# Kernel optimization log

Measured on AMD Instinct MI355X. Metric: run time of the kernel, lower is better.

The kernel has to match this reference:

```python
import jax, jax.numpy as jnp
import numpy as np


def gcn_conv(x, src, dst, W, b, num_nodes):
    # PyG GCNConv: add self-loops, symmetric deg^-1/2 normalization, scatter-add.
    h = x @ W                                    # [N, out]
    loops = jnp.arange(num_nodes, dtype=src.dtype)
    s = jnp.concatenate([src, loops])            # [E+N]
    d = jnp.concatenate([dst, loops])            # [E+N]
    deg = jax.ops.segment_sum(jnp.ones_like(d, dtype=h.dtype), d, num_segments=num_nodes)
    dinv = jnp.where(deg > 0, jax.lax.rsqrt(deg), 0.0)
    norm = dinv[s] * dinv[d]                     # [E+N]
    msgs = h[s] * norm[:, None]                  # gather + scale  [E+N, out]
    out = jax.ops.segment_sum(msgs, d, num_segments=num_nodes)
    return out + b


NUM_GRAPHS = 512


def setup_inputs() -> dict:
    key = jax.random.key(0)
    ks = jax.random.split(key, 12)
    N, E, F = 50000, 400000, 128
    x = jax.random.normal(ks[0], (N, F), dtype=jnp.float32)
    edge_index = jax.random.randint(ks[1], (2, E), 0, N, dtype=jnp.int64)
    batch = jnp.sort(jax.random.randint(ks[2], (N,), 0, NUM_GRAPHS, dtype=jnp.int64))
    def lin(k, fi, fo):
        return jax.random.normal(k, (fi, fo), dtype=jnp.float32) * (1.0 / np.sqrt(fi))
    return {
        "x": x, "edge_index": edge_index, "batch": batch,
        "W1": lin(ks[3], F, 512), "b1": jnp.zeros((512,), jnp.float32),
        "W2": lin(ks[4], 512, 256), "b2": jnp.zeros((256,), jnp.float32),
        "W3": lin(ks[5], 256, 128), "b3": jnp.zeros((128,), jnp.float32),
        "W4": lin(ks[6], 128, 32), "b4": jnp.zeros((32,), jnp.float32),
        "W5": lin(ks[7], 32, 10), "b5": jnp.zeros((10,), jnp.float32),
    }


def reference(x, edge_index, batch, W1, b1, W2, b2, W3, b3, W4, b4, W5, b5):
    N = x.shape[0]
    src, dst = edge_index[0], edge_index[1]
    h = gcn_conv(x, src, dst, W1, b1, N)
    h = jax.nn.leaky_relu(h, negative_slope=0.01)
    h = gcn_conv(h, src, dst, W2, b2, N)          # [N, 256]
    embs = jax.ops.segment_max(h, batch, num_segments=NUM_GRAPHS)  # [G, 256]
    z = ((h @ W3 + b3) @ W4 + b4) @ W5 + b5       # [N, 10]
    out = jax.ops.segment_max(z, batch, num_segments=NUM_GRAPHS)   # [G, 10]
    return (out, embs)
```

## Files before the change

### kernel.cpp

```cpp
#include <hip/hip_runtime.h>
#include <math.h>

#define DIV_UP(a,b) (((a)+(b)-1)/(b))

typedef __attribute__((ext_vector_type(8))) short bf16x8;
typedef __attribute__((ext_vector_type(4))) float f32x4;

__device__ inline unsigned short f2b(float x) {
    unsigned int u = __float_as_uint(x);
    u += 0x7fffu + ((u >> 16) & 1u);
    return (unsigned short)(u >> 16);
}

__device__ inline void cvt8(uint4 v, float* a) {
    a[0] = __uint_as_float(v.x << 16); a[1] = __uint_as_float(v.x & 0xffff0000u);
    a[2] = __uint_as_float(v.y << 16); a[3] = __uint_as_float(v.y & 0xffff0000u);
    a[4] = __uint_as_float(v.z << 16); a[5] = __uint_as_float(v.z & 0xffff0000u);
    a[6] = __uint_as_float(v.w << 16); a[7] = __uint_as_float(v.w & 0xffff0000u);
}

__device__ inline void gl16(void* lds, const void* g) {
    __builtin_amdgcn_global_load_lds(
        (const __attribute__((address_space(1))) void*)g,
        (__attribute__((address_space(3))) void*)lds, 16, 0, 0);
}

__global__ void k_zero_i(int* p, int n) {
    int i = blockIdx.x * blockDim.x + threadIdx.x;
    if (i < n) p[i] = 0;
}

__global__ void k_hist(const int* __restrict__ dst, int* __restrict__ hist, int E) {
    int i = blockIdx.x * blockDim.x + threadIdx.x;
    if (i < E) atomicAdd(&hist[dst[i]], 1);
}

__global__ __launch_bounds__(256) void k_scan_bsum(const int* __restrict__ hist,
                                                   int* __restrict__ bsum, int N) {
    __shared__ int red[256];
    int t = threadIdx.x;
    int base = blockIdx.x * 1024 + t * 4;
    int s = 0;
    if (base + 3 < N) {
        int4 v = *(const int4*)&hist[base];
        s = v.x + v.y + v.z + v.w;
    } else {
        for (int j = 0; j < 4; ++j) if (base + j < N) s += hist[base + j];
    }
    red[t] = s;
    __syncthreads();
    for (int off = 128; off >= 1; off >>= 1) {
        if (t < off) red[t] += red[t + off];
        __syncthreads();
    }
    if (t == 0) bsum[blockIdx.x] = red[0];
}

__global__ __launch_bounds__(1024) void k_scan_boff(const int* __restrict__ bsum,
        int* __restrict__ boff, int* __restrict__ row_off, int NB, int N) {
    __shared__ int s[1024];
    int t = threadIdx.x;
    int v = (t < NB) ? bsum[t] : 0;
    s[t] = v;
    __syncthreads();
    for (int off = 1; off < 1024; off <<= 1) {
        int u = (t >= off) ? s[t - off] : 0;
        __syncthreads();
        s[t] += u;
        __syncthreads();
    }
    if (t < NB) boff[t] = s[t] - v;
    if (t == NB - 1) row_off[N] = s[t];
}

__global__ __launch_bounds__(256) void k_scan_apply(const int* __restrict__ hist,
        const int* __restrict__ boff, int* __restrict__ row_off,
        float* __restrict__ dinv, int N) {
    __shared__ int s[256];
    int t = threadIdx.x;
    int base = blockIdx.x * 1024 + t * 4;
    int v[4];
    int loc = 0;
#pragma unroll
    for (int j = 0; j < 4; ++j) { v[j] = (base + j < N) ? hist[base + j] : 0; loc += v[j]; }
    s[t] = loc;
    __syncthreads();
    for (int off = 1; off < 256; off <<= 1) {
        int u = (t >= off) ? s[t - off] : 0;
        __syncthreads();
        s[t] += u;
        __syncthreads();
    }
    int run = boff[blockIdx.x] + s[t] - loc;
#pragma unroll
    for (int j = 0; j < 4; ++j) {
        if (base + j < N) {
            row_off[base + j] = run;
            dinv[base + j] = rsqrtf((float)(v[j] + 1));
        }
        run += v[j];
    }
}

__global__ void k_bin(const int* __restrict__ src, const int* __restrict__ dst,
                      const int* __restrict__ row_off, int* __restrict__ cursor,
                      const float* __restrict__ dinv,
                      int* __restrict__ csr_src, float* __restrict__ csr_w, int E) {
    int i = blockIdx.x * blockDim.x + threadIdx.x;
    if (i >= E) return;
    int d = dst[i], s = src[i];
    int pos = row_off[d] + atomicAdd(&cursor[d], 1);
    csr_src[pos] = s;
    csr_w[pos] = dinv[s] * dinv[d];
}

__global__ __launch_bounds__(256) void k_pre(
        const float* __restrict__ W3, const float* __restrict__ W4,
        const float* __restrict__ W5, const float* __restrict__ b3,
        const float* __restrict__ b4, const float* __restrict__ b5,
        float* __restrict__ WcT, float* __restrict__ bc,
        const int* __restrict__ batch, int* __restrict__ bounds, int N, int G, int nb,
        const float* __restrict__ x, unsigned short* __restrict__ xb, int n4,
        const float* __restrict__ W1, unsigned short* __restrict__ w1t, int K1, int N1,
        const float* __restrict__ W2, unsigned short* __restrict__ w2t, int K2, int N2) {
    int b = blockIdx.x;
    int t = threadIdx.x;
    if (b < 11) {
        int c = b;
        if (c < 10) {
            __shared__ float Tc[128];
            if (t < 128) {
                float s = 0.f;
#pragma unroll 8
                for (int k = 0; k < 32; ++k) s = fmaf(W4[t * 32 + k], W5[k * 10 + c], s);
                Tc[t] = s;
            }
            __syncthreads();
            float s = 0.f;
            const float* w3r = &W3[t * 128];
#pragma unroll 8
            for (int j = 0; j < 128; ++j) s = fmaf(w3r[j], Tc[j], s);
            WcT[c * 256 + t] = s;
        } else {
            __shared__ float v[32];
            if (t < 32) {
                float s = b4[t];
                for (int j = 0; j < 128; ++j) s = fmaf(b3[j], W4[j * 32 + t], s);
                v[t] = s;
            }
            __syncthreads();
            if (t < 10) {
                float s = b5[t];
                for (int k = 0; k < 32; ++k) s = fmaf(v[k], W5[k * 10 + t], s);
                bc[t] = s;
            }
        }
        return;
    }
    if (b < 11 + nb) {
        int g = (b - 11) * 256 + t;
        if (g > G) return;
        int lo = 0, hi = N;
        while (lo < hi) { int mid = (lo + hi) >> 1; if (batch[mid] < g) lo = mid + 1; else hi = mid; }
        bounds[g] = lo;
        return;
    }
    int i = (b - 11 - nb) * 256 + t;
    if (i < n4) {
        float4 v = ((const float4*)x)[i];
        ushort4 o;
        o.x = f2b(v.x); o.y = f2b(v.y); o.z = f2b(v.z); o.w = f2b(v.w);
        ((ushort4*)xb)[i] = o;
        return;
    }
    i -= n4;
    if (i < K1 * N1) {
        int k = i / N1, n = i % N1;
        w1t[(size_t)n * K1 + k] = f2b(W1[i]);
        return;
    }
    i -= K1 * N1;
    if (i < K2 * N2) {
        int k = i / N2, n = i % N2;
        w2t[(size_t)n * K2 + k] = f2b(W2[i]);
    }
}

template <int F>
__global__ __launch_bounds__(256) void k_gather_b(const unsigned short* __restrict__ H,
        const int* __restrict__ row_off, const int* __restrict__ csr_src,
        const float* __restrict__ csr_w, const float* __restrict__ dinv,
        const float* __restrict__ bias, unsigned short* __restrict__ outb, int N) {
    const int LPN = F / 8;
    const int NPB = 256 / LPN;
    int node = blockIdx.x * NPB + threadIdx.x / LPN;
    if (node >= N) return;
    int f = (threadIdx.x % LPN) * 8;
    const unsigned short* Hf = H + f;
    float sc = dinv[node]; sc *= sc;
    float a[8];
    cvt8(*(const uint4*)&Hf[(size_t)node * F], a);
#pragma unroll
    for (int j = 0; j < 8; ++j) a[j] *= sc;
    if (bias) {
#pragma unroll
        for (int j = 0; j < 8; ++j) a[j] += bias[f + j];
    }
    int e0 = row_off[node], e1 = row_off[node + 1];
    int e = e0;
    for (; e + 4 <= e1; e += 4) {
        int s0 = csr_src[e + 0], s1 = csr_src[e + 1];
        int s2 = csr_src[e + 2], s3 = csr_src[e + 3];
        uint4 v0 = *(const uint4*)&Hf[(size_t)s0 * F];
        uint4 v1 = *(const uint4*)&Hf[(size_t)s1 * F];
        uint4 v2 = *(const uint4*)&Hf[(size_t)s2 * F];
        uint4 v3 = *(const uint4*)&Hf[(size_t)s3 * F];
        float w0 = csr_w[e + 0], w1 = csr_w[e + 1];
        float w2 = csr_w[e + 2], w3 = csr_w[e + 3];
        float b0[8], b1[8], b2[8], b3[8];
        cvt8(v0, b0); cvt8(v1, b1); cvt8(v2, b2); cvt8(v3, b3);
#pragma unroll
        for (int j = 0; j < 8; ++j) {
            a[j] = fmaf(w0, b0[j], a[j]);
            a[j] = fmaf(w1, b1[j], a[j]);
            a[j] = fmaf(w2, b2[j], a[j]);
            a[j] = fmaf(w3, b3[j], a[j]);
        }
    }
    for (; e < e1; ++e) {
        int s = csr_src[e];
        float w = csr_w[e];
        float b[8];
        cvt8(*(const uint4*)&Hf[(size_t)s * F], b);
#pragma unroll
        for (int j = 0; j < 8; ++j) a[j] = fmaf(w, b[j], a[j]);
    }
    uint4 o;
    o.x = (unsigned)f2b(a[0]) | ((unsigned)f2b(a[1]) << 16);
    o.y = (unsigned)f2b(a[2]) | ((unsigned)f2b(a[3]) << 16);
    o.z = (unsigned)f2b(a[4]) | ((unsigned)f2b(a[5]) << 16);
    o.w = (unsigned)f2b(a[6]) | ((unsigned)f2b(a[7]) << 16);
    *(uint4*)&outb[(size_t)node * F + f] = o;
}

template <int OUT_BF16, int ACT>
__global__ __launch_bounds__(512) void k_gemm_mfma256(const unsigned short* __restrict__ A,
        const unsigned short* __restrict__ Bt, const float* __restrict__ bias,
        void* __restrict__ Cout, int M, int K, int NC) {
    __shared__ __align__(16) unsigned short As[128][64];
    __shared__ __align__(16) unsigned short Bs[256][64];
    int tid = threadIdx.x;
    int wave = tid >> 6, lane = tid & 63;
    int row0 = blockIdx.y * 128, col0 = blockIdx.x * 256;
    int wr = (wave >> 2) * 64, wc = (wave & 3) * 64;
    f32x4 acc[4][4] = {};
    int lr = lane & 15;
    int lg = lane >> 4;
    int sw = ((lane & 7) ^ (lane >> 3)) << 3;
    int ch0 = (lg ^ (lr & 7)) << 3;
    int ch1 = ch0 ^ (4 << 3);

    for (int k0 = 0; k0 < K; k0 += 64) {
#pragma unroll
        for (int c = 0; c < 2; ++c) {
            int rl = c * 64 + wave * 8 + (lane >> 3);
            int gr = min(row0 + rl, M - 1);
            gl16(&As[c * 64 + wave * 8][0], &A[(size_t)gr * K + k0 + sw]);
        }
#pragma unroll
        for (int c = 0; c < 4; ++c) {
            int rl = c * 64 + wave * 8 + (lane >> 3);
            gl16(&Bs[c * 64 + wave * 8][0], &Bt[(size_t)(col0 + rl) * K + k0 + sw]);
        }
        __syncthreads();
        bf16x8 af[2][4], bv[2][4];
#pragma unroll
        for (int i = 0; i < 4; ++i) {
            int ra = wr + i * 16 + lr;
            int rb = wc + i * 16 + lr;
            af[0][i] = *(const bf16x8*)&As[ra][ch0];
            af[1][i] = *(const bf16x8*)&As[ra][ch1];
            bv[0][i] = *(const bf16x8*)&Bs[rb][ch0];
            bv[1][i] = *(const bf16x8*)&Bs[rb][ch1];
        }
#pragma unroll
        for (int s = 0; s < 2; ++s)
#pragma unroll
            for (int i = 0; i < 4; ++i)
#pragma unroll
                for (int j = 0; j < 4; ++j)
                    acc[i][j] = __builtin_amdgcn_mfma_f32_16x16x32_bf16(bv[s][j], af[s][i], acc[i][j], 0, 0, 0);
        __syncthreads();
    }

    int q4 = lg * 4;
    float4 bb[4];
#pragma unroll
    for (int j = 0; j < 4; ++j)
        bb[j] = bias ? *(const float4*)&bias[col0 + wc + j * 16 + q4]
                     : make_float4(0.f, 0.f, 0.f, 0.f);
#pragma unroll
    for (int i = 0; i < 4; ++i) {
        int row = row0 + wr + i * 16 + lr;
        if (row >= M) continue;
#pragma unroll
        for (int j = 0; j < 4; ++j) {
            int c0 = col0 + wc + j * 16 + q4;
            float4 v;
            v.x = acc[i][j][0] + bb[j].x;
            v.y = acc[i][j][1] + bb[j].y;
            v.z = acc[i][j][2] + bb[j].z;
            v.w = acc[i][j][3] + bb[j].w;
            if (ACT) {
                v.x = (v.x >= 0.f) ? v.x : 0.01f * v.x;
                v.y = (v.y >= 0.f) ? v.y : 0.01f * v.y;
                v.z = (v.z >= 0.f) ? v.z : 0.01f * v.z;
                v.w = (v.w >= 0.f) ? v.w : 0.01f * v.w;
            }
            if (OUT_BF16) {
                uint2 o;
                o.x = (unsigned)f2b(v.x) | ((unsigned)f2b(v.y) << 16);
                o.y = (unsigned)f2b(v.z) | ((unsigned)f2b(v.w) << 16);
                *(uint2*)&((unsigned short*)Cout)[(size_t)row * NC + c0] = o;
            } else {
                *(float4*)&((float*)Cout)[(size_t)row * NC + c0] = v;
            }
        }
    }
}

__global__ __launch_bounds__(320) void k_head_segmax(const unsigned short* __restrict__ H,
        const float* __restrict__ WcT, const float* __restrict__ bc,
        const int* __restrict__ bounds, float* __restrict__ out,
        float* __restrict__ out_emb) {
    __shared__ __align__(16) float Ws[10][260];
    __shared__ float bs[10];
    __shared__ float red[320];
    int t = threadIdx.x;
    for (int i = t; i < 2560; i += 320) Ws[i / 256][i % 256] = WcT[i];
    if (t < 10) bs[t] = bc[t];
    __syncthreads();
    int g = blockIdx.x;
    int s = bounds[g], e = bounds[g + 1];
    int col = t % 10, rs = t / 10;
    float m = -INFINITY;
    for (int r = s + rs; r < e; r += 32) {
        const unsigned short* hr = &H[(size_t)r * 256];
        float acc = bs[col];
#pragma unroll 4
        for (int k = 0; k < 256; k += 8) {
            float h[8];
            cvt8(*(const uint4*)&hr[k], h);
            float4 wa = *(const float4*)&Ws[col][k];
            float4 wb = *(const float4*)&Ws[col][k + 4];
            acc = fmaf(h[0], wa.x, acc);
            acc = fmaf(h[1], wa.y, acc);
            acc = fmaf(h[2], wa.z, acc);
            acc = fmaf(h[3], wa.w, acc);
            acc = fmaf(h[4], wb.x, acc);
            acc = fmaf(h[5], wb.y, acc);
            acc = fmaf(h[6], wb.z, acc);
            acc = fmaf(h[7], wb.w, acc);
        }
        m = fmaxf(m, acc);
    }
    red[t] = m;
    __syncthreads();
    for (int step = 16; step >= 1; step >>= 1) {
        if (rs < step) red[rs * 10 + col] = fmaxf(red[rs * 10 + col], red[(rs + step) * 10 + col]);
        __syncthreads();
    }
    if (rs == 0) out[(size_t)g * 10 + col] = red[col];
    if (t < 256) {
        float mm = -INFINITY;
        for (int r = s; r < e; ++r)
            mm = fmaxf(mm, __uint_as_float(((unsigned)H[(size_t)r * 256 + t]) << 16));
        out_emb[(size_t)g * 256 + t] = mm;
    }
}

extern "C" void kernel_launch(void* const* d_in, const int* in_sizes, int n_in,
                              void* d_out, int out_size, void* d_ws, size_t ws_size,
                              hipStream_t stream) {
    const float* x  = (const float*)d_in[0];
    const int* ei   = (const int*)d_in[1];
    const int* batch= (const int*)d_in[2];
    const float* W1 = (const float*)d_in[3];
    const float* b1 = (const float*)d_in[4];
    const float* W2 = (const float*)d_in[5];
    const float* b2 = (const float*)d_in[6];
    const float* W3 = (const float*)d_in[7];
    const float* b3 = (const float*)d_in[8];
    const float* W4 = (const float*)d_in[9];
    const float* b4 = (const float*)d_in[10];
    const float* W5 = (const float*)d_in[11];
    const float* b5 = (const float*)d_in[12];

    const int N  = in_sizes[2];
    const int F  = in_sizes[0] / N;
    const int E  = in_sizes[1] / 2;
    const int C1 = in_sizes[4];
    const int C2 = in_sizes[6];
    const int C5 = in_sizes[12];
    const int G  = out_size / (C2 + C5);
    const int NB = DIV_UP(N, 1024);

    const int* srcp = ei;
    const int* dstp = ei + E;

    uintptr_t p = (uintptr_t)d_ws;
    auto carve = [&](size_t bytes) {
        uintptr_t r = p;
        p += (bytes + 255) & ~(size_t)255;
        return (void*)r;
    };
    int* hist    = (int*)carve(sizeof(int) * N);
    int* cursor  = (int*)carve(sizeof(int) * N);
    int* row_off = (int*)carve(sizeof(int) * (N + 1));
    int* bounds  = (int*)carve(sizeof(int) * (G + 1));
    int* bsum    = (int*)carve(sizeof(int) * NB);
    int* boff    = (int*)carve(sizeof(int) * NB);
    int* csr_src = (int*)carve(sizeof(int) * E);
    float* csr_w = (float*)carve(sizeof(float) * E);
    float* dinv  = (float*)carve(sizeof(float) * N);
    float* wct   = (float*)carve(sizeof(float) * C2 * C5);
    float* bcv   = (float*)carve(sizeof(float) * C5);
    unsigned short* w1t = (unsigned short*)carve(sizeof(short) * F * C1);
    unsigned short* w2t = (unsigned short*)carve(sizeof(short) * C1 * C2);
    unsigned short* xb    = (unsigned short*)carve(sizeof(short) * (size_t)N * F);
    unsigned short* aggxb = (unsigned short*)carve(sizeof(short) * (size_t)N * F);
    unsigned short* h1b   = (unsigned short*)carve(sizeof(short) * (size_t)N * C1);
    unsigned short* t2b   = (unsigned short*)carve(sizeof(short) * (size_t)N * C2);
    unsigned short* h2b   = (unsigned short*)carve(sizeof(short) * (size_t)N * C2);

    float* out     = (float*)d_out;
    float* out_emb = out + (size_t)G * C5;

    int zspan = (int)(((sizeof(int) * N + 255) & ~(size_t)255) / 4) + N;
    k_zero_i<<<DIV_UP(zspan, 256), 256, 0, stream>>>(hist, zspan);
    k_hist<<<DIV_UP(E, 256), 256, 0, stream>>>(dstp, hist, E);
    k_scan_bsum<<<NB, 256, 0, stream>>>(hist, bsum, N);
    k_scan_boff<<<1, 1024, 0, stream>>>(bsum, boff, row_off, NB, N);
    k_scan_apply<<<NB, 256, 0, stream>>>(hist, boff, row_off, dinv, N);
    k_bin<<<DIV_UP(E, 256), 256, 0, stream>>>(srcp, dstp, row_off, cursor, dinv,
                                              csr_src, csr_w, E);

    int n4 = N * F / 4;
    int nb_bounds = DIV_UP(G + 1, 256);
    int prep_total = n4 + F * C1 + C1 * C2;
    int pre_blocks = 11 + nb_bounds + DIV_UP(prep_total, 256);
    k_pre<<<pre_blocks, 256, 0, stream>>>(W3, W4, W5, b3, b4, b5, wct, bcv,
                                          batch, bounds, N, G, nb_bounds,
                                          x, xb, n4, W1, w1t, F, C1, W2, w2t, C1, C2);

    k_gather_b<128><<<DIV_UP(N, 16), 256, 0, stream>>>(
        xb, row_off, csr_src, csr_w, dinv, nullptr, aggxb, N);
    dim3 g1(C1 / 256, DIV_UP(N, 128));
    k_gemm_mfma256<1, 1><<<g1, 512, 0, stream>>>(aggxb, w1t, b1, h1b, N, F, C1);

    dim3 g2(C2 / 256, DIV_UP(N, 128));
    k_gemm_mfma256<1, 0><<<g2, 512, 0, stream>>>(h1b, w2t, nullptr, t2b, N, C1, C2);
    k_gather_b<256><<<DIV_UP(N, 8), 256, 0, stream>>>(
        t2b, row_off, csr_src, csr_w, dinv, b2, h2b, N);

    k_head_segmax<<<G, 320, 0, stream>>>(h2b, wct, bcv, bounds, out, out_emb);
}
```

Before: 286.8 us.

## Fuse second aggregation with head projection and segment-max via float atomics

Merges the layer-2 gather, the collapsed W3·W4·W5 head projection and both segment-max reductions into one kernel. Each block of 8 nodes computes h2 in registers, runs the 10-column head with shuffle reductions, and pushes per-graph maxima to the outputs with sign-aware integer atomic max/min. The separate bf16 h2 buffer write/read, the graph-bounds binary search and the per-graph head kernel are dropped, and the output is initialised to -inf in the prep kernel instead. The cost is many global atomics, each block reloading the head weights into LDS, and h2 being kept in fp32 instead of rounded to bf16, which changes numerics slightly.

```diff
diff --git a/kernel.cpp b/kernel.cpp
--- a/kernel.cpp
+++ b/kernel.cpp
@@ -17,6 +17,11 @@
     a[2] = __uint_as_float(v.y << 16); a[3] = __uint_as_float(v.y & 0xffff0000u);
     a[4] = __uint_as_float(v.z << 16); a[5] = __uint_as_float(v.z & 0xffff0000u);
     a[6] = __uint_as_float(v.w << 16); a[7] = __uint_as_float(v.w & 0xffff0000u);
+}
+
+__device__ inline void atomicMaxF(float* addr, float v) {
+    if (v >= 0.f) atomicMax((int*)addr, __float_as_int(v));
+    else          atomicMin((unsigned int*)addr, __float_as_uint(v));
 }
 
 __device__ inline void gl16(void* lds, const void* g) {
@@ -119,7 +124,7 @@
         const float* __restrict__ W5, const float* __restrict__ b3,
         const float* __restrict__ b4, const float* __restrict__ b5,
         float* __restrict__ WcT, float* __restrict__ bc,
-        const int* __restrict__ batch, int* __restrict__ bounds, int N, int G, int nb,
+        unsigned* __restrict__ outp, int nout, int nfo,
         const float* __restrict__ x, unsigned short* __restrict__ xb, int n4,
         const float* __restrict__ W1, unsigned short* __restrict__ w1t, int K1, int N1,
         const float* __restrict__ W2, unsigned short* __restrict__ w2t, int K2, int N2) {
@@ -157,15 +162,12 @@
         }
         return;
     }
-    if (b < 11 + nb) {
-        int g = (b - 11) * 256 + t;
-        if (g > G) return;
-        int lo = 0, hi = N;
-        while (lo < hi) { int mid = (lo + hi) >> 1; if (batch[mid] < g) lo = mid + 1; else hi = mid; }
-        bounds[g] = lo;
+    if (b < 11 + nfo) {
+        int i = (b - 11) * 256 + t;
+        if (i < nout) outp[i] = 0xff800000u;
         return;
     }
-    int i = (b - 11 - nb) * 256 + t;
+    int i = (b - 11 - nfo) * 256 + t;
     if (i < n4) {
         float4 v = ((const float4*)x)[i];
         ushort4 o;
@@ -241,6 +243,123 @@
     o.z = (unsigned)f2b(a[4]) | ((unsigned)f2b(a[5]) << 16);
     o.w = (unsigned)f2b(a[6]) | ((unsigned)f2b(a[7]) << 16);
     *(uint4*)&outb[(size_t)node * F + f] = o;
+}
+
+__global__ __launch_bounds__(256) void k_gather_head(
+        const unsigned short* __restrict__ H,
+        const int* __restrict__ row_off, const int* __restrict__ csr_src,
+        const float* __restrict__ csr_w, const float* __restrict__ dinv,
+        const float* __restrict__ bias, const int* __restrict__ batch,
+        const float* __restrict__ WcT, const float* __restrict__ bc,
+        float* __restrict__ out, float* __restrict__ out_emb, int N) {
+    __shared__ __align__(16) float Ws[10][260];
+    __shared__ float bs[10];
+    __shared__ __align__(16) float h2s[8][264];
+    __shared__ float zl[8][10];
+    __shared__ int gl[8];
+    int t = threadIdx.x;
+    for (int i = t; i < 2560; i += 256) Ws[i >> 8][i & 255] = WcT[i];
+    if (t < 10) bs[t] = bc[t];
+    int nl = t >> 5;
+    int q  = t & 31;
+    int node = blockIdx.x * 8 + nl;
+    bool valid = node < N;
+    if (q == 0) gl[nl] = valid ? batch[node] : -1;
+    int f = q * 8;
+    const unsigned short* Hf = H + f;
+    float a[8] = {0.f, 0.f, 0.f, 0.f, 0.f, 0.f, 0.f, 0.f};
+    if (valid) {
+        float sc = dinv[node]; sc *= sc;
+        cvt8(*(const uint4*)&Hf[(size_t)node * 256], a);
+#pragma unroll
+        for (int j = 0; j < 8; ++j) a[j] = fmaf(a[j], sc, bias[f + j]);
+        int e0 = row_off[node], e1 = row_off[node + 1];
+        int e = e0;
+        for (; e + 4 <= e1; e += 4) {
+            int s0 = csr_src[e + 0], s1 = csr_src[e + 1];
+            int s2 = csr_src[e + 2], s3 = csr_src[e + 3];
+            uint4 v0 = *(const uint4*)&Hf[(size_t)s0 * 256];
+            uint4 v1 = *(const uint4*)&Hf[(size_t)s1 * 256];
+            uint4 v2 = *(const uint4*)&Hf[(size_t)s2 * 256];
+            uint4 v3 = *(const uint4*)&Hf[(size_t)s3 * 256];
+            float w0 = csr_w[e + 0], w1 = csr_w[e + 1];
+            float w2 = csr_w[e + 2], w3 = csr_w[e + 3];
+            float b0[8], b1[8], b2v[8], b3v[8];
+            cvt8(v0, b0); cvt8(v1, b1); cvt8(v2, b2v); cvt8(v3, b3v);
+#pragma unroll
+            for (int j = 0; j < 8; ++j) {
+                a[j] = fmaf(w0, b0[j], a[j]);
+                a[j] = fmaf(w1, b1[j], a[j]);
+                a[j] = fmaf(w2, b2v[j], a[j]);
+                a[j] = fmaf(w3, b3v[j], a[j]);
+            }
+        }
+        for (; e < e1; ++e) {
+            int s = csr_src[e];
+            float w = csr_w[e];
+            float bv[8];
+            cvt8(*(const uint4*)&Hf[(size_t)s * 256], bv);
+#pragma unroll
+            for (int j = 0; j < 8; ++j) a[j] = fmaf(w, bv[j], a[j]);
+        }
+    }
+    __syncthreads();
+
+#pragma unroll
+    for (int c = 0; c < 10; ++c) {
+        float4 wa = *(const float4*)&Ws[c][f];
+        float4 wb = *(const float4*)&Ws[c][f + 4];
+        float s = a[0] * wa.x;
+        s = fmaf(a[1], wa.y, s);
+        s = fmaf(a[2], wa.z, s);
+        s = fmaf(a[3], wa.w, s);
+        s = fmaf(a[4], wb.x, s);
+        s = fmaf(a[5], wb.y, s);
+        s = fmaf(a[6], wb.z, s);
+        s = fmaf(a[7], wb.w, s);
+        s += __shfl_xor(s, 16);
+        s += __shfl_xor(s, 8);
+        s += __shfl_xor(s, 4);
+        s += __shfl_xor(s, 2);
+        s += __shfl_xor(s, 1);
+        if (q == 0) zl[nl][c] = s + bs[c];
+    }
+    *(float4*)&h2s[nl][f]     = make_float4(a[0], a[1], a[2], a[3]);
+    *(float4*)&h2s[nl][f + 4] = make_float4(a[4], a[5], a[6], a[7]);
+    __syncthreads();
+
+    {
+        int curg = -1; float m = 0.f;
+#pragma unroll
+        for (int n = 0; n < 8; ++n) {
+            int g = gl[n];
+            if (g < 0) continue;
+            float v = h2s[n][t];
+            if (g != curg) {
+                if (curg >= 0) atomicMaxF(&out_emb[(size_t)curg * 256 + t], m);
+                curg = g; m = v;
+            } else {
+                m = fmaxf(m, v);
+            }
+        }
+        if (curg >= 0) atomicMaxF(&out_emb[(size_t)curg * 256 + t], m);
+    }
+    if (t < 10) {
+        int curg = -1; float m = 0.f;
+#pragma unroll
+        for (int n = 0; n < 8; ++n) {
+            int g = gl[n];
+            if (g < 0) continue;
+            float v = zl[n][t];
+            if (g != curg) {
+                if (curg >= 0) atomicMaxF(&out[(size_t)curg * 10 + t], m);
+                curg = g; m = v;
+            } else {
+                m = fmaxf(m, v);
+            }
+        }
+        if (curg >= 0) atomicMaxF(&out[(size_t)curg * 10 + t], m);
+    }
 }
 
 template <int OUT_BF16, int ACT>
@@ -329,56 +448,6 @@
     }
 }
 
-__global__ __launch_bounds__(320) void k_head_segmax(const unsigned short* __restrict__ H,
-        const float* __restrict__ WcT, const float* __restrict__ bc,
-        const int* __restrict__ bounds, float* __restrict__ out,
-        float* __restrict__ out_emb) {
-    __shared__ __align__(16) float Ws[10][260];
-    __shared__ float bs[10];
-    __shared__ float red[320];
-    int t = threadIdx.x;
-    for (int i = t; i < 2560; i += 320) Ws[i / 256][i % 256] = WcT[i];
-    if (t < 10) bs[t] = bc[t];
-    __syncthreads();
-    int g = blockIdx.x;
-    int s = bounds[g], e = bounds[g + 1];
-    int col = t % 10, rs = t / 10;
-    float m = -INFINITY;
-    for (int r = s + rs; r < e; r += 32) {
-        const unsigned short* hr = &H[(size_t)r * 256];
-        float acc = bs[col];
-#pragma unroll 4
-        for (int k = 0; k < 256; k += 8) {
-            float h[8];
-            cvt8(*(const uint4*)&hr[k], h);
-            float4 wa = *(const float4*)&Ws[col][k];
-            float4 wb = *(const float4*)&Ws[col][k + 4];
-            acc = fmaf(h[0], wa.x, acc);
-            acc = fmaf(h[1], wa.y, acc);
-            acc = fmaf(h[2], wa.z, acc);
-            acc = fmaf(h[3], wa.w, acc);
-            acc = fmaf(h[4], wb.x, acc);
-            acc = fmaf(h[5], wb.y, acc);
-            acc = fmaf(h[6], wb.z, acc);
-            acc = fmaf(h[7], wb.w, acc);
-        }
-        m = fmaxf(m, acc);
-    }
-    red[t] = m;
-    __syncthreads();
-    for (int step = 16; step >= 1; step >>= 1) {
-        if (rs < step) red[rs * 10 + col] = fmaxf(red[rs * 10 + col], red[(rs + step) * 10 + col]);
-        __syncthreads();
-    }
-    if (rs == 0) out[(size_t)g * 10 + col] = red[col];
-    if (t < 256) {
-        float mm = -INFINITY;
-        for (int r = s; r < e; ++r)
-            mm = fmaxf(mm, __uint_as_float(((unsigned)H[(size_t)r * 256 + t]) << 16));
-        out_emb[(size_t)g * 256 + t] = mm;
-    }
-}
-
 extern "C" void kernel_launch(void* const* d_in, const int* in_sizes, int n_in,
                               void* d_out, int out_size, void* d_ws, size_t ws_size,
                               hipStream_t stream) {
@@ -417,7 +486,6 @@
     int* hist    = (int*)carve(sizeof(int) * N);
     int* cursor  = (int*)carve(sizeof(int) * N);
     int* row_off = (int*)carve(sizeof(int) * (N + 1));
-    int* bounds  = (int*)carve(sizeof(int) * (G + 1));
     int* bsum    = (int*)carve(sizeof(int) * NB);
     int* boff    = (int*)carve(sizeof(int) * NB);
     int* csr_src = (int*)carve(sizeof(int) * E);
@@ -431,7 +499,6 @@
     unsigned short* aggxb = (unsigned short*)carve(sizeof(short) * (size_t)N * F);
     unsigned short* h1b   = (unsigned short*)carve(sizeof(short) * (size_t)N * C1);
     unsigned short* t2b   = (unsigned short*)carve(sizeof(short) * (size_t)N * C2);
-    unsigned short* h2b   = (unsigned short*)carve(sizeof(short) * (size_t)N * C2);
 
     float* out     = (float*)d_out;
     float* out_emb = out + (size_t)G * C5;
@@ -446,11 +513,12 @@
                                               csr_src, csr_w, E);
 
     int n4 = N * F / 4;
-    int nb_bounds = DIV_UP(G + 1, 256);
+    int nout = G * (C2 + C5);
+    int nfo = DIV_UP(nout, 256);
     int prep_total = n4 + F * C1 + C1 * C2;
-    int pre_blocks = 11 + nb_bounds + DIV_UP(prep_total, 256);
+    int pre_blocks = 11 + nfo + DIV_UP(prep_total, 256);
     k_pre<<<pre_blocks, 256, 0, stream>>>(W3, W4, W5, b3, b4, b5, wct, bcv,
-                                          batch, bounds, N, G, nb_bounds,
+                                          (unsigned*)d_out, nout, nfo,
                                           x, xb, n4, W1, w1t, F, C1, W2, w2t, C1, C2);
 
     k_gather_b<128><<<DIV_UP(N, 16), 256, 0, stream>>>(
@@ -460,8 +528,8 @@
 
     dim3 g2(C2 / 256, DIV_UP(N, 128));
     k_gemm_mfma256<1, 0><<<g2, 512, 0, stream>>>(h1b, w2t, nullptr, t2b, N, C1, C2);
-    k_gather_b<256><<<DIV_UP(N, 8), 256, 0, stream>>>(
-        t2b, row_off, csr_src, csr_w, dinv, b2, h2b, N);
-
-    k_head_segmax<<<G, 320, 0, stream>>>(h2b, wct, bcv, bounds, out, out_emb);
-}
+
+    k_gather_head<<<DIV_UP(N, 8), 256, 0, stream>>>(
+        t2b, row_off, csr_src, csr_w, dinv, b2, batch, wct, bcv,
+        out, out_emb, N);
+}
```

New measurement: 274.2 us. 1.05x faster.
